# Optimization experiments

Measured on AMD Instinct MI355X. Metric: run time of the kernel, lower is better.

## Reference

```python
import jax, jax.numpy as jnp
import numpy as np
from jax import lax

B, L = 16384, 32
HID, CIN = 8, 2
N_SUB = 2            # RK4 substeps per spline interval (fixed-step stand-in for torchcde's adaptive solver)
T10_LO, T10_HI = 0.1, 7.0


def push_zeros(a):
    # torch: move nonzero entries of each row to the right end, zeros to the left.
    # stable ascending sort on validity key (0 for zeros, 1 for valid) reproduces this exactly
    # because the invalid entries are exactly 0.
    keys = (a != 0).astype(jnp.int32)
    order = jnp.argsort(keys, axis=1)  # jax sorts are stable
    return jnp.take_along_axis(a, order, axis=1)


def setup_inputs() -> dict:
    key = jax.random.key(0)
    ks = jax.random.split(key, 12)
    fa_len = jax.random.randint(ks[0], (B, 1), L // 2, L + 1)          # 16..32 valid points
    valid = jnp.arange(L)[None, :] < fa_len                             # (B, L)
    X_fa_in = jnp.where(valid, jax.random.uniform(ks[1], (B, L), minval=0.1, maxval=1.1), 0.0)
    fa_vals_in = jnp.where(valid, jax.random.uniform(ks[2], (B, L), minval=0.05, maxval=0.45), 0.0)
    TR_vals = jax.random.uniform(ks[3], (B, 1), minval=0.003, maxval=0.01)
    fa_mask = valid

    def lin(k, fout, fin):
        kw, kb = jax.random.split(k)
        s = 1.0 / np.sqrt(fin)
        return (jax.random.uniform(kw, (fout, fin), minval=-s, maxval=s),
                jax.random.uniform(kb, (fout,), minval=-s, maxval=s))

    W_init, b_init = lin(ks[4], HID, CIN)        # self.initial: Linear(2, 8)
    W1, b1 = lin(ks[5], 256, HID)                # CDE_Func.linear1
    W2, b2 = lin(ks[6], CIN * HID, 256)          # CDE_Func.linear2
    Wr1, br1 = lin(ks[7], 200, HID)              # reg_T10
    Wr2, br2 = lin(ks[8], 200, 200)
    Wr3, br3 = lin(ks[9], 1, 200)
    return dict(X_fa_in=X_fa_in, fa_vals_in=fa_vals_in, TR_vals=TR_vals,
                W_init=W_init, b_init=b_init, W1=W1, b1=b1, W2=W2, b2=b2,
                Wr1=Wr1, br1=br1, Wr2=Wr2, br2=br2, Wr3=Wr3, br3=br3,
                fa_mask=fa_mask, fa_len=fa_len)


def _forward(X_fa_in, fa_vals_in, TR_vals, W_init, b_init, W1, b1, W2, b2,
             Wr1, br1, Wr2, br2, Wr3, br3, fa_mask, fa_len):
    fl = fa_len[:, 0]                       # (B,) int
    fl_f = fl.astype(X_fa_in.dtype)
    mean = jnp.sum(X_fa_in, axis=1) / fl_f
    Xn = X_fa_in / mean[:, None]
    X_fa = push_zeros(Xn)
    fa_vals = push_zeros(fa_vals_in)
    bidx = jnp.arange(X_fa.shape[0])
    last_X = X_fa[bidx, fl - 1][:, None]            # pushed array indexed at fa_len-1 (as in torch)
    last_fa = fa_vals_in[bidx, fl - 1][:, None]     # original array indexed at fa_len-1
    X_fa = jnp.where(X_fa == 0.0, last_X, X_fa)
    fa_vals = jnp.where(fa_vals == 0.0, last_fa, fa_vals)
    x = jnp.stack([fa_vals, X_fa], axis=-1)         # (B, L, 2): channels (fa, X)

    # Hermite cubic with backward differences, unit knot spacing t_i = i
    diffs = x[:, 1:] - x[:, :-1]                    # (B, L-1, C)
    m = jnp.concatenate([diffs[:, :1], diffs], axis=1)  # m_0 = fwd diff, m_i = backward diff
    X0s, X1s = x[:, :-1], x[:, 1:]                  # per-interval knot values (B, L-1, C)
    M0s, M1s = m[:, :-1], m[:, 1:]

    z0 = x[:, 0] @ W_init.T + b_init                # X.evaluate(interval[0]) == first knot

    def f(z):  # CDE vector field: (B, HID) -> (B, HID, CIN)
        h = jax.nn.relu(z @ W1.T + b1)
        g = jnp.tanh(h @ W2.T + b2)
        return g.reshape(z.shape[0], HID, CIN)

    hstep = 1.0 / N_SUB
    nI = x.shape[1] - 1
    intervals = jnp.repeat(jnp.arange(nI), N_SUB)
    s0s = jnp.tile(jnp.arange(N_SUB) * hstep, nI).astype(x.dtype)

    def step(z, ts):
        i, s0 = ts
        x0, x1 = X0s[:, i], X1s[:, i]
        m0, m1 = M0s[:, i], M1s[:, i]

        def dX(s):  # spline derivative dX/dt at local coord s in [0,1]
            s2 = s * s
            return ((6 * s2 - 6 * s) * x0 + (3 * s2 - 4 * s + 1) * m0 +
                    (-6 * s2 + 6 * s) * x1 + (3 * s2 - 2 * s) * m1)

        def F(s, zz):
            return jnp.einsum('bhc,bc->bh', f(zz), dX(s))

        k1 = F(s0, z)
        k2 = F(s0 + hstep / 2, z + 0.5 * hstep * k1)
        k3 = F(s0 + hstep / 2, z + 0.5 * hstep * k2)
        k4 = F(s0 + hstep, z + hstep * k3)
        return z + (hstep / 6) * (k1 + 2 * k2 + 2 * k3 + k4), None

    z_T, _ = lax.scan(step, z0, (intervals, s0s))

    h1 = jax.nn.gelu(z_T @ Wr1.T + br1, approximate=False)
    h2 = jax.nn.gelu(h1 @ Wr2.T + br2, approximate=False)
    t = (h2 @ Wr3.T + br3)[:, 0]
    T10 = T10_LO + jax.nn.sigmoid(t)[:, None] * (T10_HI - T10_LO)   # (B, 1)
    R1 = 1.0 / T10
    E = jnp.exp(-TR_vals * R1)                                      # (B, 1)
    X_out = (1 - E) * jnp.sin(fa_vals_in) / (1 - jnp.cos(fa_vals_in) * E)
    mean2 = jnp.sum(X_out, axis=1) / fl_f
    X_out = X_out / mean2[:, None]
    M0 = jnp.ones_like(T10)
    return X_out, T10, M0


def reference(X_fa_in, fa_vals_in, TR_vals, W_init, b_init, W1, b1, W2, b2,
              Wr1, br1, Wr2, br2, Wr3, br3, fa_mask, fa_len):
    return _forward(X_fa_in, fa_vals_in, TR_vals, W_init, b_init, W1, b1, W2, b2,
                    Wr1, br1, Wr2, br2, Wr3, br3, fa_mask, fa_len)
```

## Files before the change

kernel.cpp:

```cpp
#include <hip/hip_runtime.h>
#include <hip/hip_bf16.h>

#define B_ROWS 16384
#define L_SEQ  32

typedef _Float16 f16;
typedef __attribute__((ext_vector_type(4))) _Float16 f16x4;
typedef __attribute__((ext_vector_type(8))) _Float16 f16x8;
typedef __attribute__((ext_vector_type(4))) float f32x4;
typedef __attribute__((ext_vector_type(4))) unsigned int u32x4;

__device__ __forceinline__ unsigned pkh(float a, float b) {
    return __builtin_bit_cast(unsigned, __builtin_amdgcn_cvt_pkrtz(a, b));
}
__device__ __forceinline__ float tanh_fast(float x) {
    float e = __expf(2.0f * x);
    float r = __builtin_amdgcn_rcpf(e + 1.0f);
    return fmaf(-2.0f, r, 1.0f);
}
__device__ __forceinline__ float gelu_exact(float x) {
    return 0.5f * x * (1.0f + erff(x * 0.70710678118654752440f));
}
__device__ __forceinline__ void pin2(uint2& v) {
    unsigned x0 = v.x, x1 = v.y;
    asm volatile("" : "+v"(x0), "+v"(x1));
    v = make_uint2(x0, x1);
}
__device__ __forceinline__ void pin4(u32x4& v) {
    unsigned x0 = v[0], x1 = v[1], x2 = v[2], x3 = v[3];
    asm volatile("" : "+v"(x0), "+v"(x1), "+v"(x2), "+v"(x3));
    v = (u32x4){x0, x1, x2, x3};
}

__global__ __launch_bounds__(256, 2) void fused_kernel(
    const float* __restrict__ Xin, const float* __restrict__ Fin,
    const float* __restrict__ TRv,
    const int*   __restrict__ fa_len,
    const float* __restrict__ Wi,  const float* __restrict__ bi,
    const float* __restrict__ W1g, const float* __restrict__ b1g,
    const float* __restrict__ W2g, const float* __restrict__ b2g,
    const float* __restrict__ Wr1, const float* __restrict__ br1,
    const float* __restrict__ Wr2, const float* __restrict__ br2,
    const float* __restrict__ Wr3, const float* __restrict__ br3,
    float* __restrict__ out)
{
    __shared__ __align__(16) float xm[32 * 132];
#define XM(r_, i_, c_) xm[(r_) * 132 + (i_) * 4 + (c_)]

    const int tid = threadIdx.x;
    const int g16 = tid >> 4, sub = tid & 15;

    float mean_r[2]; int fl_r[2];
#pragma unroll
    for (int r = 0; r < 2; ++r) {
        const int row_l = g16 * 2 + r;
        const int row   = blockIdx.x * 32 + row_l;
        const float* Xr = Xin + row * L_SEQ;
        const float* Fr = Fin + row * L_SEQ;
        float xr0 = Xr[sub], xr1 = Xr[sub + 16];
        float fr0 = Fr[sub], fr1 = Fr[sub + 16];
        fl_r[r] = fa_len[row];
        float s = xr0 + xr1;
        s += __shfl_xor(s, 1, 16);
        s += __shfl_xor(s, 2, 16);
        s += __shfl_xor(s, 4, 16);
        s += __shfl_xor(s, 8, 16);
        mean_r[r] = s / (float)fl_r[r];
        XM(row_l, sub, 0)      = fr0; XM(row_l, sub, 1)      = xr0;
        XM(row_l, sub + 16, 0) = fr1; XM(row_l, sub + 16, 1) = xr1;
    }
    __syncthreads();

    float ff[2][2], xf[2][2];
#pragma unroll
    for (int r = 0; r < 2; ++r) {
        const int row_l = g16 * 2 + r;
        const int fl = fl_r[r];
        const float mean = mean_r[r];
        const int shift = L_SEQ - fl;
        int lsrc  = fl - 1 - shift;
        int lsrcC = lsrc < 0 ? 0 : lsrc;
        float lastX = (lsrc >= 0) ? (XM(row_l, lsrcC, 1) / mean) : 0.0f;
        float lastF = XM(row_l, fl - 1, 0);
#pragma unroll
        for (int u = 0; u < 2; ++u) {
            int p = sub + u * 16;
            int src = p - shift;
            int sc  = src < 0 ? 0 : src;
            float fraw = XM(row_l, sc, 0);
            float xraw = XM(row_l, sc, 1);
            ff[r][u] = (src >= 0) ? fraw : lastF;
            xf[r][u] = (src >= 0) ? (xraw / mean) : lastX;
        }
    }
    __syncthreads();
#pragma unroll
    for (int r = 0; r < 2; ++r) {
        const int row_l = g16 * 2 + r;
#pragma unroll
        for (int u = 0; u < 2; ++u) {
            int p = sub + u * 16;
            XM(row_l, p, 0) = ff[r][u];
            XM(row_l, p, 1) = xf[r][u];
        }
    }
    __syncthreads();
#pragma unroll
    for (int r = 0; r < 2; ++r) {
        const int row_l = g16 * 2 + r;
#pragma unroll
        for (int u = 0; u < 2; ++u) {
            int p = sub + u * 16;
            int qd = (p == 0) ? 1 : p;
            XM(row_l, p, 2) = XM(row_l, qd, 0) - XM(row_l, qd - 1, 0);
            XM(row_l, p, 3) = XM(row_l, qd, 1) - XM(row_l, qd - 1, 1);
        }
    }
    __syncthreads();

    const int wv   = tid >> 6;
    const int lane = tid & 63;
    const int n    = lane & 15;
    const int q    = lane >> 4;
    const int nr   = n & 7;
    const int rowl = wv * 8 + nr;
    const int rowg = blockIdx.x * 32 + rowl;

    uint2 a1[16];
#pragma unroll
    for (int t = 0; t < 16; ++t) {
        const float* wr = W1g + (t * 16 + n) * 8 + (q < 2 ? q * 4 : 0);
        float4 w4 = *(const float4*)wr;
        float b1v = b1g[t * 16 + n];
        unsigned d0 = (q < 2) ? pkh(w4.x, w4.y) : (q == 2 ? pkh(b1v, 0.0f) : 0u);
        unsigned d1 = (q < 2) ? pkh(w4.z, w4.w) : 0u;
        a1[t] = make_uint2(d0, d1);
        pin2(a1[t]);
    }
    u32x4 a2[8];
#pragma unroll
    for (int kk = 0; kk < 8; ++kk) {
        const float* w2r = W2g + n * 256 + kk * 32 + 4 * q;
        float4 p0 = *(const float4*)(w2r);
        float4 p1 = *(const float4*)(w2r + 16);
        a2[kk] = (u32x4){pkh(p0.x, p0.y), pkh(p0.z, p0.w), pkh(p1.x, p1.y), pkh(p1.z, p1.w)};
        pin4(a2[kk]);
    }
    f32x4 c2seed;
#pragma unroll
    for (int r = 0; r < 4; ++r) c2seed[r] = b2g[4 * q + r];

    float f0 = XM(rowl, 0, 0), X0 = XM(rowl, 0, 1);
    float z0 = fmaf(Wi[(2 * q) * 2], f0, fmaf(Wi[(2 * q) * 2 + 1], X0, bi[2 * q]));
    float z1 = fmaf(Wi[(2 * q + 1) * 2], f0, fmaf(Wi[(2 * q + 1) * 2 + 1], X0, bi[2 * q + 1]));

    const int bpi = (((q & 1) << 5) + n) << 2;
    const f32x4 zero4 = {0.f, 0.f, 0.f, 0.f};
    const f16x8 zf16 = {0, 0, 0, 0, 0, 0, 0, 0};

    auto make_bz = [&](float zza, float zzb) -> uint2 {
        unsigned myz = pkh(zza, zzb);
        int b0 = __builtin_amdgcn_ds_bpermute(bpi, (int)myz);
        int b1 = __builtin_amdgcn_ds_bpermute(bpi + 64, (int)myz);
        unsigned bz0 = (q < 2) ? (unsigned)b0 : (q == 2 ? 0x3C00u : 0u);
        unsigned bz1 = (q < 2) ? (unsigned)b1 : 0u;
        return make_uint2(bz0, bz1);
    };

    auto FEVAL = [&](float zza, float zzb, float d0c, float d1c, float& ko0, float& ko1) {
        uint2 bzp = make_bz(zza, zzb);
        f16x4 bz = __builtin_bit_cast(f16x4, bzp);

        f32x4 c1[16];
#pragma unroll
        for (int t = 0; t < 16; ++t)
            c1[t] = __builtin_amdgcn_mfma_f32_16x16x16f16(
                __builtin_bit_cast(f16x4, a1[t]), bz, zero4, 0, 0, 0);

        f16x8 hf[8];
#pragma unroll
        for (int kk = 0; kk < 8; ++kk) {
            u32x4 w = (u32x4){pkh(c1[2 * kk][0],     c1[2 * kk][1]),
                              pkh(c1[2 * kk][2],     c1[2 * kk][3]),
                              pkh(c1[2 * kk + 1][0], c1[2 * kk + 1][1]),
                              pkh(c1[2 * kk + 1][2], c1[2 * kk + 1][3])};
            hf[kk] = __builtin_elementwise_max(__builtin_bit_cast(f16x8, w), zf16);
        }

        f32x4 c2a = c2seed, c2b = zero4;
#pragma unroll
        for (int kk = 0; kk < 4; ++kk) {
            c2a = __builtin_amdgcn_mfma_f32_16x16x32_f16(
                __builtin_bit_cast(f16x8, a2[kk]), hf[kk], c2a, 0, 0, 0);
            c2b = __builtin_amdgcn_mfma_f32_16x16x32_f16(
                __builtin_bit_cast(f16x8, a2[kk + 4]), hf[kk + 4], c2b, 0, 0, 0);
        }
        f32x4 G = c2a + c2b;

        float t0 = tanh_fast(G[0]), t1 = tanh_fast(G[1]);
        float t2 = tanh_fast(G[2]), t3 = tanh_fast(G[3]);
        ko0 = fmaf(t0, d0c, t1 * d1c);
        ko1 = fmaf(t2, d0c, t3 * d1c);
    };

#pragma unroll 1
    for (int i = 0; i < 31; ++i) {
        float4 P0 = *(const float4*)&XM(rowl, i, 0);
        float4 P1 = *(const float4*)&XM(rowl, i + 1, 0);
        float m0f = P0.z, m0X = P0.w, m1f = P1.z, m1X = P1.w;
        float df  = P0.x - P1.x, dXx = P0.y - P1.y;

        float d25f = fmaf(-1.125f, df,  fmaf(0.1875f, m0f, -0.3125f * m1f));
        float d25X = fmaf(-1.125f, dXx, fmaf(0.1875f, m0X, -0.3125f * m1X));
        float d50f = fmaf(-1.5f,   df,  fmaf(-0.25f,  m0f, -0.25f   * m1f));
        float d50X = fmaf(-1.5f,   dXx, fmaf(-0.25f,  m0X, -0.25f   * m1X));
        float d75f = fmaf(-1.125f, df,  fmaf(-0.3125f, m0f, 0.1875f * m1f));
        float d75X = fmaf(-1.125f, dXx, fmaf(-0.3125f, m0X, 0.1875f * m1X));

#pragma unroll 1
        for (int ssi = 0; ssi < 2; ++ssi) {
            float daf = ssi ? d50f : m0f,  daX = ssi ? d50X : m0X;
            float dbf = ssi ? d75f : d25f, dbX = ssi ? d75X : d25X;
            float ddf = ssi ? m1f  : d50f, ddX = ssi ? m1X  : d50X;

            float k1a, k1b, k2a, k2b, k3a, k3b, k4a, k4b, zza, zzb;
            FEVAL(z0, z1, daf, daX, k1a, k1b);
            zza = fmaf(0.25f, k1a, z0); zzb = fmaf(0.25f, k1b, z1);
            FEVAL(zza, zzb, dbf, dbX, k2a, k2b);
            zza = fmaf(0.25f, k2a, z0); zzb = fmaf(0.25f, k2b, z1);
            FEVAL(zza, zzb, dbf, dbX, k3a, k3b);
            zza = fmaf(0.5f, k3a, z0);  zzb = fmaf(0.5f, k3b, z1);
            FEVAL(zza, zzb, ddf, ddX, k4a, k4b);

            float ka = fmaf(2.f, k2a, k1a); ka = fmaf(2.f, k3a, ka);
            float kb = fmaf(2.f, k2b, k1b); kb = fmaf(2.f, k3b, kb);
            z0 = fmaf(1.f / 12.f, ka + k4a, z0);
            z1 = fmaf(1.f / 12.f, kb + k4b, z1);
        }
    }

    uint2 bzp = make_bz(z0, z1);
    f16x4 bzr = __builtin_bit_cast(f16x4, bzp);
    f32x4 c1r[13];
#pragma unroll
    for (int t = 0; t < 13; ++t) {
        int m = 16 * t + n;
        uint2 afp = make_uint2(0u, 0u);
        if (q < 2) {
            if (m < 200) {
                float4 w4 = *(const float4*)(Wr1 + m * 8 + 4 * q);
                afp = make_uint2(pkh(w4.x, w4.y), pkh(w4.z, w4.w));
            }
        } else if (q == 2) {
            float b = (m < 200) ? br1[m] : 0.0f;
            afp.x = pkh(b, 0.0f);
        }
        c1r[t] = __builtin_amdgcn_mfma_f32_16x16x16f16(
            __builtin_bit_cast(f16x4, afp), bzr, zero4, 0, 0, 0);
    }

    f16x8 hf2[7];
#pragma unroll
    for (int kk = 0; kk < 7; ++kk) {
        float g0 = gelu_exact(c1r[2 * kk][0]), g1 = gelu_exact(c1r[2 * kk][1]);
        float g2 = gelu_exact(c1r[2 * kk][2]), g3 = gelu_exact(c1r[2 * kk][3]);
        float g4 = 0.f, g5 = 0.f, g6 = 0.f, g7 = 0.f;
        if (kk < 6) {
            g4 = gelu_exact(c1r[2 * kk + 1][0]); g5 = gelu_exact(c1r[2 * kk + 1][1]);
            g6 = gelu_exact(c1r[2 * kk + 1][2]); g7 = gelu_exact(c1r[2 * kk + 1][3]);
        }
        u32x4 w = (u32x4){pkh(g0, g1), pkh(g2, g3), pkh(g4, g5), pkh(g6, g7)};
        hf2[kk] = __builtin_bit_cast(f16x8, w);
    }

    float tpart = 0.0f;
#pragma unroll 1
    for (int mt = 0; mt < 13; ++mt) {
        int mb = 16 * mt + 4 * q;
        f32x4 c2 = zero4;
        if (mb + 3 < 200) c2 = *(const f32x4*)(br2 + mb);
        int m2 = 16 * mt + n;
#pragma unroll
        for (int kk = 0; kk < 7; ++kk) {
            u32x4 af = {0u, 0u, 0u, 0u};
            if (m2 < 200) {
                int k0 = 32 * kk + 4 * q;
                const float* wr = Wr2 + m2 * 200 + k0;
                if (k0 + 3 < 200) {
                    float4 wa = *(const float4*)(wr);
                    af[0] = pkh(wa.x, wa.y); af[1] = pkh(wa.z, wa.w);
                }
                if (k0 + 19 < 200) {
                    float4 wb = *(const float4*)(wr + 16);
                    af[2] = pkh(wb.x, wb.y); af[3] = pkh(wb.z, wb.w);
                }
            }
            c2 = __builtin_amdgcn_mfma_f32_16x16x32_f16(
                __builtin_bit_cast(f16x8, af), hf2[kk], c2, 0, 0, 0);
        }
        float4 w3 = make_float4(0.f, 0.f, 0.f, 0.f);
        if (mb + 3 < 200) w3 = *(const float4*)(Wr3 + mb);
        tpart = fmaf(w3.x, gelu_exact(c2[0]), tpart);
        tpart = fmaf(w3.y, gelu_exact(c2[1]), tpart);
        tpart = fmaf(w3.z, gelu_exact(c2[2]), tpart);
        tpart = fmaf(w3.w, gelu_exact(c2[3]), tpart);
    }
    tpart += __shfl_xor(tpart, 16);
    tpart += __shfl_xor(tpart, 32);

    float tval = tpart + br3[0];
    float sig  = __fdividef(1.0f, 1.0f + __expf(-tval));
    float T10  = 0.1f + 6.9f * sig;
    float E    = __expf(-TRv[rowg] * __builtin_amdgcn_rcpf(T10));

    const float* Fr = Fin + rowg * 32 + 8 * q;
    float xo[8]; float ssum = 0.0f;
#pragma unroll
    for (int j = 0; j < 8; ++j) {
        float fa = Fr[j];
        float sn = __sinf(fa), cs = __cosf(fa);
        float v = __fdividef((1.0f - E) * sn, 1.0f - cs * E);
        xo[j] = v; ssum += v;
    }
    ssum += __shfl_xor(ssum, 16);
    ssum += __shfl_xor(ssum, 32);
    float mean2 = ssum / (float)fa_len[rowg];
    float inv   = __fdividef(1.0f, mean2);

    if (n < 8) {
        float4* dst = (float4*)(out + rowg * 32 + 8 * q);
        dst[0] = make_float4(xo[0] * inv, xo[1] * inv, xo[2] * inv, xo[3] * inv);
        dst[1] = make_float4(xo[4] * inv, xo[5] * inv, xo[6] * inv, xo[7] * inv);
        if (q == 0) {
            out[B_ROWS * L_SEQ + rowg] = T10;
            out[B_ROWS * L_SEQ + B_ROWS + rowg] = 1.0f;
        }
    }
#undef XM
}

extern "C" void kernel_launch(void* const* d_in, const int* in_sizes, int n_in,
                              void* d_out, int out_size, void* d_ws, size_t ws_size,
                              hipStream_t stream) {
    const float* Xin  = (const float*)d_in[0];
    const float* Fin  = (const float*)d_in[1];
    const float* TRv  = (const float*)d_in[2];
    const float* Wi   = (const float*)d_in[3];
    const float* bi   = (const float*)d_in[4];
    const float* W1g  = (const float*)d_in[5];
    const float* b1g  = (const float*)d_in[6];
    const float* W2g  = (const float*)d_in[7];
    const float* b2g  = (const float*)d_in[8];
    const float* Wr1  = (const float*)d_in[9];
    const float* br1  = (const float*)d_in[10];
    const float* Wr2  = (const float*)d_in[11];
    const float* br2  = (const float*)d_in[12];
    const float* Wr3  = (const float*)d_in[13];
    const float* br3  = (const float*)d_in[14];
    const int*   flen = (const int*)d_in[16];

    float* outp = (float*)d_out;
    (void)d_ws; (void)ws_size;

    fused_kernel<<<dim3(B_ROWS / 32), dim3(256), 0, stream>>>(
        Xin, Fin, TRv, flen, Wi, bi, W1g, b1g, W2g, b2g,
        Wr1, br1, Wr2, br2, Wr3, br3, outp);
}
```

Measured before the change: 279.7 us.

## Split hidden dimension across wave pairs with LDS exchange per CDE evaluation

Previously each wave handled 8 rows using 16-column MFMA tiles, so half of every tile was duplicated work. Now two waves form a pair covering 16 distinct rows, and each wave computes half of the 256-wide hidden layer. The partial second-layer sums are combined through shared memory with a block-wide barrier on every function evaluation, and the regression head's second layer is split the same way. Redundant MFMA work and register pressure go down, at the cost of 248 barriers per block inside the RK4 loop, which may serialize the waves.

```diff
diff --git a/kernel.cpp b/kernel.cpp
--- a/kernel.cpp
+++ b/kernel.cpp
@@ -45,6 +45,8 @@
     float* __restrict__ out)
 {
     __shared__ __align__(16) float xm[32 * 132];
+    __shared__ __align__(16) f32x4 exch[2][2][2][64];
+    __shared__ float texch[2][2][16];
 #define XM(r_, i_, c_) xm[(r_) * 132 + (i_) * 4 + (c_)]
 
     const int tid = threadIdx.x;
@@ -120,35 +122,38 @@
 
     const int wv   = tid >> 6;
     const int lane = tid & 63;
+    const int pairId = wv >> 1;
+    const int half   = wv & 1;
     const int n    = lane & 15;
     const int q    = lane >> 4;
-    const int nr   = n & 7;
-    const int rowl = wv * 8 + nr;
+    const int rowl = pairId * 16 + n;
     const int rowg = blockIdx.x * 32 + rowl;
 
-    uint2 a1[16];
-#pragma unroll
-    for (int t = 0; t < 16; ++t) {
+    uint2 a1[8];
+#pragma unroll
+    for (int tt = 0; tt < 8; ++tt) {
+        const int t = 8 * half + tt;
         const float* wr = W1g + (t * 16 + n) * 8 + (q < 2 ? q * 4 : 0);
         float4 w4 = *(const float4*)wr;
         float b1v = b1g[t * 16 + n];
         unsigned d0 = (q < 2) ? pkh(w4.x, w4.y) : (q == 2 ? pkh(b1v, 0.0f) : 0u);
         unsigned d1 = (q < 2) ? pkh(w4.z, w4.w) : 0u;
-        a1[t] = make_uint2(d0, d1);
-        pin2(a1[t]);
-    }
-    u32x4 a2[8];
-#pragma unroll
-    for (int kk = 0; kk < 8; ++kk) {
+        a1[tt] = make_uint2(d0, d1);
+        pin2(a1[tt]);
+    }
+    u32x4 a2[4];
+#pragma unroll
+    for (int tt = 0; tt < 4; ++tt) {
+        const int kk = 4 * half + tt;
         const float* w2r = W2g + n * 256 + kk * 32 + 4 * q;
         float4 p0 = *(const float4*)(w2r);
         float4 p1 = *(const float4*)(w2r + 16);
-        a2[kk] = (u32x4){pkh(p0.x, p0.y), pkh(p0.z, p0.w), pkh(p1.x, p1.y), pkh(p1.z, p1.w)};
-        pin4(a2[kk]);
+        a2[tt] = (u32x4){pkh(p0.x, p0.y), pkh(p0.z, p0.w), pkh(p1.x, p1.y), pkh(p1.z, p1.w)};
+        pin4(a2[tt]);
     }
     f32x4 c2seed;
 #pragma unroll
-    for (int r = 0; r < 4; ++r) c2seed[r] = b2g[4 * q + r];
+    for (int r = 0; r < 4; ++r) c2seed[r] = (half == 0) ? b2g[4 * q + r] : 0.0f;
 
     float f0 = XM(rowl, 0, 0), X0 = XM(rowl, 0, 1);
     float z0 = fmaf(Wi[(2 * q) * 2], f0, fmaf(Wi[(2 * q) * 2 + 1], X0, bi[2 * q]));
@@ -167,35 +172,41 @@
         return make_uint2(bz0, bz1);
     };
 
-    auto FEVAL = [&](float zza, float zzb, float d0c, float d1c, float& ko0, float& ko1) {
+    auto FEVAL = [&](int ph, float zza, float zzb, float d0c, float d1c,
+                     float& ko0, float& ko1) {
         uint2 bzp = make_bz(zza, zzb);
         f16x4 bz = __builtin_bit_cast(f16x4, bzp);
 
-        f32x4 c1[16];
-#pragma unroll
-        for (int t = 0; t < 16; ++t)
-            c1[t] = __builtin_amdgcn_mfma_f32_16x16x16f16(
-                __builtin_bit_cast(f16x4, a1[t]), bz, zero4, 0, 0, 0);
-
-        f16x8 hf[8];
-#pragma unroll
-        for (int kk = 0; kk < 8; ++kk) {
-            u32x4 w = (u32x4){pkh(c1[2 * kk][0],     c1[2 * kk][1]),
-                              pkh(c1[2 * kk][2],     c1[2 * kk][3]),
-                              pkh(c1[2 * kk + 1][0], c1[2 * kk + 1][1]),
-                              pkh(c1[2 * kk + 1][2], c1[2 * kk + 1][3])};
-            hf[kk] = __builtin_elementwise_max(__builtin_bit_cast(f16x8, w), zf16);
+        f32x4 c1[8];
+#pragma unroll
+        for (int tt = 0; tt < 8; ++tt)
+            c1[tt] = __builtin_amdgcn_mfma_f32_16x16x16f16(
+                __builtin_bit_cast(f16x4, a1[tt]), bz, zero4, 0, 0, 0);
+
+        f16x8 hf[4];
+#pragma unroll
+        for (int tt = 0; tt < 4; ++tt) {
+            u32x4 w = (u32x4){pkh(c1[2 * tt][0],     c1[2 * tt][1]),
+                              pkh(c1[2 * tt][2],     c1[2 * tt][3]),
+                              pkh(c1[2 * tt + 1][0], c1[2 * tt + 1][1]),
+                              pkh(c1[2 * tt + 1][2], c1[2 * tt + 1][3])};
+            hf[tt] = __builtin_elementwise_max(__builtin_bit_cast(f16x8, w), zf16);
         }
 
         f32x4 c2a = c2seed, c2b = zero4;
-#pragma unroll
-        for (int kk = 0; kk < 4; ++kk) {
-            c2a = __builtin_amdgcn_mfma_f32_16x16x32_f16(
-                __builtin_bit_cast(f16x8, a2[kk]), hf[kk], c2a, 0, 0, 0);
-            c2b = __builtin_amdgcn_mfma_f32_16x16x32_f16(
-                __builtin_bit_cast(f16x8, a2[kk + 4]), hf[kk + 4], c2b, 0, 0, 0);
-        }
-        f32x4 G = c2a + c2b;
+        c2a = __builtin_amdgcn_mfma_f32_16x16x32_f16(
+            __builtin_bit_cast(f16x8, a2[0]), hf[0], c2a, 0, 0, 0);
+        c2b = __builtin_amdgcn_mfma_f32_16x16x32_f16(
+            __builtin_bit_cast(f16x8, a2[2]), hf[2], c2b, 0, 0, 0);
+        c2a = __builtin_amdgcn_mfma_f32_16x16x32_f16(
+            __builtin_bit_cast(f16x8, a2[1]), hf[1], c2a, 0, 0, 0);
+        c2b = __builtin_amdgcn_mfma_f32_16x16x32_f16(
+            __builtin_bit_cast(f16x8, a2[3]), hf[3], c2b, 0, 0, 0);
+        f32x4 Gp = c2a + c2b;
+
+        exch[pairId][ph][half][lane] = Gp;
+        __syncthreads();
+        f32x4 G = Gp + exch[pairId][ph][half ^ 1][lane];
 
         float t0 = tanh_fast(G[0]), t1 = tanh_fast(G[1]);
         float t2 = tanh_fast(G[2]), t3 = tanh_fast(G[3]);
@@ -203,6 +214,7 @@
         ko1 = fmaf(t2, d0c, t3 * d1c);
     };
 
+    int ph = 0;
 #pragma unroll 1
     for (int i = 0; i < 31; ++i) {
         float4 P0 = *(const float4*)&XM(rowl, i, 0);
@@ -224,13 +236,13 @@
             float ddf = ssi ? m1f  : d50f, ddX = ssi ? m1X  : d50X;
 
             float k1a, k1b, k2a, k2b, k3a, k3b, k4a, k4b, zza, zzb;
-            FEVAL(z0, z1, daf, daX, k1a, k1b);
+            FEVAL(ph, z0, z1, daf, daX, k1a, k1b);       ph ^= 1;
             zza = fmaf(0.25f, k1a, z0); zzb = fmaf(0.25f, k1b, z1);
-            FEVAL(zza, zzb, dbf, dbX, k2a, k2b);
+            FEVAL(ph, zza, zzb, dbf, dbX, k2a, k2b);     ph ^= 1;
             zza = fmaf(0.25f, k2a, z0); zzb = fmaf(0.25f, k2b, z1);
-            FEVAL(zza, zzb, dbf, dbX, k3a, k3b);
+            FEVAL(ph, zza, zzb, dbf, dbX, k3a, k3b);     ph ^= 1;
             zza = fmaf(0.5f, k3a, z0);  zzb = fmaf(0.5f, k3b, z1);
-            FEVAL(zza, zzb, ddf, ddX, k4a, k4b);
+            FEVAL(ph, zza, zzb, ddf, ddX, k4a, k4b);     ph ^= 1;
 
             float ka = fmaf(2.f, k2a, k1a); ka = fmaf(2.f, k3a, ka);
             float kb = fmaf(2.f, k2b, k1b); kb = fmaf(2.f, k3b, kb);
@@ -274,8 +286,9 @@
     }
 
     float tpart = 0.0f;
+    const int mt0 = half * 7, mt1 = half ? 13 : 7;
 #pragma unroll 1
-    for (int mt = 0; mt < 13; ++mt) {
+    for (int mt = mt0; mt < mt1; ++mt) {
         int mb = 16 * mt + 4 * q;
         f32x4 c2 = zero4;
         if (mb + 3 < 200) c2 = *(const f32x4*)(br2 + mb);
@@ -307,8 +320,10 @@
     }
     tpart += __shfl_xor(tpart, 16);
     tpart += __shfl_xor(tpart, 32);
-
-    float tval = tpart + br3[0];
+    if (lane < 16) texch[pairId][half][n] = tpart;
+    __syncthreads();
+    float tval = texch[pairId][0][n] + texch[pairId][1][n] + br3[0];
+
     float sig  = __fdividef(1.0f, 1.0f + __expf(-tval));
     float T10  = 0.1f + 6.9f * sig;
     float E    = __expf(-TRv[rowg] * __builtin_amdgcn_rcpf(T10));
@@ -327,7 +342,7 @@
     float mean2 = ssum / (float)fa_len[rowg];
     float inv   = __fdividef(1.0f, mean2);
 
-    if (n < 8) {
+    if (half == 0) {
         float4* dst = (float4*)(out + rowg * 32 + 8 * q);
         dst[0] = make_float4(xo[0] * inv, xo[1] * inv, xo[2] * inv, xo[3] * inv);
         dst[1] = make_float4(xo[4] * inv, xo[5] * inv, xo[6] * inv, xo[7] * inv);
```

After: 244.5 us. 12.6% less time.
